# Performance work log

Measured on AMD Instinct MI355X. Metric: run time of the kernel, lower is better.

Reference implementation:

```python
import jax, jax.numpy as jnp
import numpy as np

HIDDEN, FFN, N_EXPERTS, TOP_K = 1024, 2816, 8, 2


def setup_inputs() -> dict:
    key = jax.random.key(0)
    k1, k2, k3, k4, k5 = jax.random.split(key, 5)
    hidden_states = jax.random.normal(k1, (1, 2048, HIDDEN), dtype=jnp.float32)
    # torch Linear weights: [out, in]; experts stacked on leading E axis
    Wgate = jax.random.normal(k2, (N_EXPERTS, HIDDEN), dtype=jnp.float32) * 0.02
    Wg = jax.random.normal(k3, (N_EXPERTS, FFN, HIDDEN), dtype=jnp.float32) * 0.02
    Wu = jax.random.normal(k4, (N_EXPERTS, FFN, HIDDEN), dtype=jnp.float32) * 0.02
    Wd = jax.random.normal(k5, (N_EXPERTS, HIDDEN, FFN), dtype=jnp.float32) * 0.02
    return {"hidden_states": hidden_states, "Wgate": Wgate, "Wg": Wg, "Wu": Wu, "Wd": Wd}


def reference(hidden_states, Wgate, Wg, Wu, Wd):
    x = hidden_states.reshape(-1, hidden_states.shape[-1])  # [T, H]
    # --- router ---
    logits = jnp.einsum('th,eh->te', x, Wgate)               # [T, E]
    weights = jax.nn.softmax(logits, axis=-1)
    topk_w, topk_i = jax.lax.top_k(weights, TOP_K)           # [T, K]
    topk_w = topk_w / jnp.sum(topk_w, axis=-1, keepdims=True)
    # per-token per-expert combine weight (zero if expert not in top-k)
    comb = jnp.sum(jax.nn.one_hot(topk_i, N_EXPERTS, dtype=x.dtype) * topk_w[..., None], axis=1)  # [T, E]
    # --- all-expert SwiGLU (dense reference for the gather-compute-scatter loop) ---
    g = jnp.einsum('th,efh->tef', x, Wg)                     # [T, E, F]
    u = jnp.einsum('th,efh->tef', x, Wu)
    h = jax.nn.silu(g) * u
    y = jnp.einsum('tef,ehf->teh', h, Wd)                    # [T, E, H]
    out = jnp.einsum('te,teh->th', comb, y)                  # [T, H]
    return out
```

## Files before the change

kernel.cpp:

```cpp
#include <hip/hip_runtime.h>
#include <hip/hip_bf16.h>

#define HIDDEN 1024
#define FFN    2816
#define NEXP   8
#define NTOK   2048

typedef __attribute__((ext_vector_type(8))) short short8;
typedef __attribute__((ext_vector_type(4))) short bf16x4;
typedef __attribute__((ext_vector_type(4))) float f32x4;

static __device__ __forceinline__ short f2bf(float f) {
    __hip_bfloat16 h = __float2bfloat16(f);
    return *(short*)&h;
}

static __device__ __forceinline__ void gl_lds16(const short* g, short* l) {
    __builtin_amdgcn_global_load_lds(
        (const __attribute__((address_space(1))) void*)g,
        (__attribute__((address_space(3))) void*)l, 16, 0, 0);
}

#define WAITV(N) asm volatile("s_waitcnt vmcnt(" #N ")" ::: "memory")
#define BAR()    do { __builtin_amdgcn_s_barrier(); \
                      __builtin_amdgcn_sched_barrier(0); } while (0)

static __device__ __forceinline__ void
router_body(int t, int lane, const float* __restrict__ x,
            const float* __restrict__ Wgate, int* __restrict__ counts,
            int* __restrict__ tok, float* __restrict__ wts)
{
    float acc[NEXP];
#pragma unroll
    for (int e = 0; e < NEXP; e++) acc[e] = 0.f;
    const float* xrow = x + (size_t)t * HIDDEN;
    for (int h = lane; h < HIDDEN; h += 64) {
        float xv = xrow[h];
#pragma unroll
        for (int e = 0; e < NEXP; e++) acc[e] += xv * Wgate[e * HIDDEN + h];
    }
#pragma unroll
    for (int off = 32; off > 0; off >>= 1) {
#pragma unroll
        for (int e = 0; e < NEXP; e++) acc[e] += __shfl_down(acc[e], off);
    }
    if (lane == 0) {
        float mx = acc[0];
#pragma unroll
        for (int e = 1; e < NEXP; e++) mx = fmaxf(mx, acc[e]);
        float p[NEXP];
#pragma unroll
        for (int e = 0; e < NEXP; e++) p[e] = __expf(acc[e] - mx);
        int i0 = 0; float p0 = p[0];
#pragma unroll
        for (int e = 1; e < NEXP; e++) if (p[e] > p0) { p0 = p[e]; i0 = e; }
        int i1 = -1; float p1 = -1.f;
#pragma unroll
        for (int e = 0; e < NEXP; e++) {
            if (e == i0) continue;
            if (p[e] > p1) { p1 = p[e]; i1 = e; }
        }
        float inv = 1.f / (p0 + p1);
        float w0 = p0 * inv, w1 = p1 * inv;
        int s0 = atomicAdd(&counts[i0], 1);
        tok[i0 * NTOK + s0] = t; wts[i0 * NTOK + s0] = w0;
        int s1 = atomicAdd(&counts[i1], 1);
        tok[i1 * NTOK + s1] = t; wts[i1 * NTOK + s1] = w1;
    }
}

__global__ void __launch_bounds__(64)
router_kernel(const float* __restrict__ x, const float* __restrict__ Wgate,
              int* __restrict__ counts, int* __restrict__ tok,
              float* __restrict__ wts)
{
    router_body(blockIdx.x, threadIdx.x, x, Wgate, counts, tok, wts);
}

#define N04  ((long long)NTOK * HIDDEN / 4)
#define NW4  ((long long)NEXP * FFN * HIDDEN / 4)
#define CVTA_BLOCKS 11776
__global__ void __launch_bounds__(256)
cvt_xgu_router(const float* __restrict__ x, const float* __restrict__ Wgate,
               int* __restrict__ counts, int* __restrict__ tok,
               float* __restrict__ wts,
               const float* __restrict__ s1, const float* __restrict__ s2,
               short* __restrict__ d0, short* __restrict__ d1,
               short* __restrict__ d2)
{
    int bid = blockIdx.x;
    int tid = threadIdx.x;
    if (bid < 512) {
        int t = bid * 4 + (tid >> 6);
        router_body(t, tid & 63, x, Wgate, counts, tok, wts);
        return;
    }
    long long base4 = (long long)(bid - 512) * 1024;
#pragma unroll
    for (int p = 0; p < 4; p++) {
        long long i = base4 + p * 256 + tid;
        const float* s; short* d; long long r;
        if (i < N04)            { s = x;  d = d0; r = i; }
        else if (i < N04 + NW4) { s = s1; d = d1; r = i - N04; }
        else                    { s = s2; d = d2; r = i - N04 - NW4; }
        float4 a = ((const float4*)s)[r];
        bf16x4 o;
        o[0] = f2bf(a.x); o[1] = f2bf(a.y); o[2] = f2bf(a.z); o[3] = f2bf(a.w);
        *(bf16x4*)(d + 4 * r) = o;
    }
}

#define FFN1_BLOCKS 2816
#define CVTD_BLOCKS 2048
__global__ void __launch_bounds__(256, 2)
ffn1_v6(const short* __restrict__ xbf, const short* __restrict__ Wgbf,
        const short* __restrict__ Wubf, const int* __restrict__ counts,
        const int* __restrict__ tok, short* __restrict__ hbuf,
        const float* __restrict__ Wd, short* __restrict__ wdbf)
{
    int bid = blockIdx.x;
    int tid = threadIdx.x;
    if (bid >= FFN1_BLOCKS) {
        long long base4 = (long long)(bid - FFN1_BLOCKS) * 2816;
#pragma unroll
        for (int p = 0; p < 11; p++) {
            long long r = base4 + p * 256 + tid;
            float4 a = ((const float4*)Wd)[r];
            bf16x4 o;
            o[0] = f2bf(a.x); o[1] = f2bf(a.y); o[2] = f2bf(a.z); o[3] = f2bf(a.w);
            *(bf16x4*)(wdbf + 4 * r) = o;
        }
        return;
    }
    int xb  = bid / 176;
    int yz  = bid - xb * 176;
    int e   = yz / 22;
    int fb  = yz - e * 22;
    int cnt = counts[e];
    int row0 = xb * 128;
    if (row0 >= cnt) return;
    int off_e = 0;
#pragma unroll
    for (int i = 0; i < NEXP; i++) if (i < e) off_e += counts[i];
    int f0 = fb * 128;

    __shared__ short Xs[3][128 * 32];
    __shared__ short Gs[3][128 * 32];
    __shared__ short Us[3][128 * 32];
    __shared__ int   stok[128];

    if (tid < 128) stok[tid] = tok[e * NTOK + min(row0 + tid, cnt - 1)];
    __syncthreads();

    int lane = tid & 63, w = tid >> 6;
    int l15 = lane & 15, lq = lane >> 4;
    int wm = (w & 1) * 64, wn = (w >> 1) * 64;

    int prow   = lane >> 2;
    int gchunk = (lane & 3) ^ ((lane >> 3) & 3);
    const short* xsrc[2]; const short* gsrc[2]; const short* usrc[2];
    int rb[2];
#pragma unroll
    for (int j = 0; j < 2; j++) {
        int rbase = w * 32 + j * 16;
        int r = rbase + prow;
        xsrc[j] = xbf + (size_t)stok[r] * HIDDEN + gchunk * 8;
        gsrc[j] = Wgbf + (size_t)e * FFN * HIDDEN + (size_t)(f0 + r) * HIDDEN + gchunk * 8;
        usrc[j] = Wubf + (size_t)e * FFN * HIDDEN + (size_t)(f0 + r) * HIDDEN + gchunk * 8;
        rb[j] = rbase * 32;
    }

    int aoff[4], boff[4];
#pragma unroll
    for (int mi = 0; mi < 4; mi++) {
        int r = wm + mi * 16 + l15;
        aoff[mi] = r * 32 + (lq ^ ((r >> 1) & 3)) * 8;
    }
#pragma unroll
    for (int ni = 0; ni < 4; ni++) {
        int r = wn + ni * 16 + l15;
        boff[ni] = r * 32 + (lq ^ ((r >> 1) & 3)) * 8;
    }

    f32x4 cg[4][4], cu[4][4];
#pragma unroll
    for (int i = 0; i < 4; i++)
#pragma unroll
        for (int j = 0; j < 4; j++) { cg[i][j] = (f32x4)0.f; cu[i][j] = (f32x4)0.f; }

#define STAGE1(B, T) do { int _k = (T) * 32;                       \
    _Pragma("unroll")                                              \
    for (int j = 0; j < 2; j++) {                                  \
        gl_lds16(xsrc[j] + _k, &Xs[B][rb[j]]);                     \
        gl_lds16(gsrc[j] + _k, &Gs[B][rb[j]]);                     \
        gl_lds16(usrc[j] + _k, &Us[B][rb[j]]);                     \
    } } while (0)

#define COMP1(B) do {                                              \
    short8 af[4], bg[4], bu[4];                                    \
    _Pragma("unroll")                                              \
    for (int mi = 0; mi < 4; mi++)                                 \
        af[mi] = *(const short8*)&Xs[B][aoff[mi]];                 \
    _Pragma("unroll")                                              \
    for (int ni = 0; ni < 4; ni++) {                               \
        bg[ni] = *(const short8*)&Gs[B][boff[ni]];                 \
        bu[ni] = *(const short8*)&Us[B][boff[ni]];                 \
    }                                                              \
    _Pragma("unroll")                                              \
    for (int mi = 0; mi < 4; mi++)                                 \
    _Pragma("unroll")                                              \
    for (int ni = 0; ni < 4; ni++) {                               \
        cg[mi][ni] = __builtin_amdgcn_mfma_f32_16x16x32_bf16(af[mi], bg[ni], cg[mi][ni], 0, 0, 0); \
        cu[mi][ni] = __builtin_amdgcn_mfma_f32_16x16x32_bf16(af[mi], bu[ni], cu[mi][ni], 0, 0, 0); \
    } } while (0)

    STAGE1(0, 0); STAGE1(1, 1); STAGE1(2, 2);

    for (int tt = 0; tt < 30; tt += 3) {
        WAITV(12); BAR(); COMP1(0); BAR(); STAGE1(0, tt + 3);
        WAITV(12); BAR(); COMP1(1); BAR(); STAGE1(1, tt + 4);
        WAITV(12); BAR(); COMP1(2); BAR(); if (tt + 5 < 32) STAGE1(2, tt + 5);
    }
    WAITV(6);  BAR(); COMP1(0);
    WAITV(0);  BAR(); COMP1(1);

#undef STAGE1
#undef COMP1

#pragma unroll
    for (int mi = 0; mi < 4; mi++)
#pragma unroll
        for (int r = 0; r < 4; r++) {
            int row = wm + mi * 16 + lq * 4 + r;
            int grow = row0 + row;
            if (grow < cnt) {
                short* hrow = hbuf + (size_t)(off_e + grow) * FFN + f0 + wn;
#pragma unroll
                for (int ni = 0; ni < 4; ni++) {
                    float g = cg[mi][ni][r], u = cu[mi][ni][r];
                    float h = g / (1.f + __expf(-g)) * u;
                    hrow[ni * 16 + l15] = f2bf(h);
                }
            }
        }
}

__global__ void __launch_bounds__(256, 2)
ffn2_v6(const short* __restrict__ hbuf, const short* __restrict__ Wdbf,
        const int* __restrict__ counts, const int* __restrict__ tok,
        const float* __restrict__ wts, float* __restrict__ out)
{
    int bid = blockIdx.x;
    int xb  = bid >> 7;
    int yz  = bid & 127;
    int e   = yz >> 4;
    int y   = yz & 15;
    int cnt = counts[e];
    int row0 = xb * 128;
    if (row0 >= cnt) return;
    int off_e = 0;
#pragma unroll
    for (int i = 0; i < NEXP; i++) if (i < e) off_e += counts[i];
    int h0    = (y >> 1) * 128;
    int kbase = (y & 1) * (FFN / 2);

    __shared__ short Hs[3][128 * 32];
    __shared__ short Ds[3][128 * 32];
    __shared__ int   stok[128];
    __shared__ float swt[128];

    int tid = threadIdx.x;
    if (tid < 128) {
        int rc = min(row0 + tid, cnt - 1);
        stok[tid] = tok[e * NTOK + rc];
        swt[tid]  = wts[e * NTOK + rc];
    }
    __syncthreads();

    int lane = tid & 63, w = tid >> 6;
    int l15 = lane & 15, lq = lane >> 4;
    int wm = (w & 1) * 64, wn = (w >> 1) * 64;

    int prow   = lane >> 2;
    int gchunk = (lane & 3) ^ ((lane >> 3) & 3);
    const short* hsrc[2]; const short* dsrc[2];
    int rb[2];
#pragma unroll
    for (int j = 0; j < 2; j++) {
        int rbase = w * 32 + j * 16;
        int r = rbase + prow;
        hsrc[j] = hbuf + (size_t)(off_e + min(row0 + r, cnt - 1)) * FFN + kbase + gchunk * 8;
        dsrc[j] = Wdbf + (size_t)e * HIDDEN * FFN + (size_t)(h0 + r) * FFN + kbase + gchunk * 8;
        rb[j] = rbase * 32;
    }

    int aoff[4], boff[4];
#pragma unroll
    for (int mi = 0; mi < 4; mi++) {
        int r = wm + mi * 16 + l15;
        aoff[mi] = r * 32 + (lq ^ ((r >> 1) & 3)) * 8;
    }
#pragma unroll
    for (int ni = 0; ni < 4; ni++) {
        int r = wn + ni * 16 + l15;
        boff[ni] = r * 32 + (lq ^ ((r >> 1) & 3)) * 8;
    }

    f32x4 c[4][4];
#pragma unroll
    for (int i = 0; i < 4; i++)
#pragma unroll
        for (int j = 0; j < 4; j++) c[i][j] = (f32x4)0.f;

#define STAGE2(B, T) do { int _k = (T) * 32;                       \
    _Pragma("unroll")                                              \
    for (int j = 0; j < 2; j++) {                                  \
        gl_lds16(hsrc[j] + _k, &Hs[B][rb[j]]);                     \
        gl_lds16(dsrc[j] + _k, &Ds[B][rb[j]]);                     \
    } } while (0)

#define COMP2(B) do {                                              \
    short8 af[4], bd[4];                                           \
    _Pragma("unroll")                                              \
    for (int mi = 0; mi < 4; mi++)                                 \
        af[mi] = *(const short8*)&Hs[B][aoff[mi]];                 \
    _Pragma("unroll")                                              \
    for (int ni = 0; ni < 4; ni++)                                 \
        bd[ni] = *(const short8*)&Ds[B][boff[ni]];                 \
    _Pragma("unroll")                                              \
    for (int mi = 0; mi < 4; mi++)                                 \
    _Pragma("unroll")                                              \
    for (int ni = 0; ni < 4; ni++)                                 \
        c[mi][ni] = __builtin_amdgcn_mfma_f32_16x16x32_bf16(af[mi], bd[ni], c[mi][ni], 0, 0, 0); \
    } while (0)

    STAGE2(0, 0); STAGE2(1, 1); STAGE2(2, 2);

    for (int tt = 0; tt < 42; tt += 3) {
        WAITV(8); BAR(); COMP2(0); BAR(); STAGE2(0, tt + 3);
        WAITV(8); BAR(); COMP2(1); BAR(); STAGE2(1, tt + 4);
        WAITV(8); BAR(); COMP2(2); BAR(); if (tt + 5 < 44) STAGE2(2, tt + 5);
    }
    WAITV(4); BAR(); COMP2(0);
    WAITV(0); BAR(); COMP2(1);

#undef STAGE2
#undef COMP2

#pragma unroll
    for (int mi = 0; mi < 4; mi++)
#pragma unroll
        for (int r = 0; r < 4; r++) {
            int row = wm + mi * 16 + lq * 4 + r;
            int grow = row0 + row;
            if (grow < cnt) {
                int t = stok[row];
                float wgt = swt[row];
                float* orow = out + (size_t)t * HIDDEN + h0 + wn;
#pragma unroll
                for (int ni = 0; ni < 4; ni++)
                    atomicAdd(&orow[ni * 16 + l15], wgt * c[mi][ni][r]);
            }
        }
}

#define LDW 40
__global__ void __launch_bounds__(256, 2)
ffn1_fb(const float* __restrict__ x, const float* __restrict__ Wg,
        const float* __restrict__ Wu, const int* __restrict__ counts,
        const int* __restrict__ tok, __hip_bfloat16* __restrict__ hbuf)
{
    int e = blockIdx.z;
    int cnt = counts[e];
    int row0 = blockIdx.x * 128;
    if (row0 >= cnt) return;
    int off_e = 0;
#pragma unroll
    for (int i = 0; i < NEXP; i++) if (i < e) off_e += counts[i];
    int f0 = blockIdx.y * 64;

    __shared__ short Xs[128][LDW];
    __shared__ short Gs[64][LDW];
    __shared__ short Us[64][LDW];
    __shared__ int   stok[128];

    int tid = threadIdx.x;
    if (tid < 128) stok[tid] = tok[e * NTOK + min(row0 + tid, cnt - 1)];
    __syncthreads();

    int lane = tid & 63, w = tid >> 6;
    int wm = (w & 1) * 64, wn = (w >> 1) * 32;
    int l15 = lane & 15, lq = lane >> 4;

    f32x4 cg[4][2], cu[4][2];
#pragma unroll
    for (int i = 0; i < 4; i++)
#pragma unroll
        for (int j = 0; j < 2; j++) { cg[i][j] = (f32x4)0.f; cu[i][j] = (f32x4)0.f; }

    const float* Wge = Wg + (size_t)e * FFN * HIDDEN;
    const float* Wue = Wu + (size_t)e * FFN * HIDDEN;

    int xr[4], xc[4]; const float* xp[4];
#pragma unroll
    for (int i = 0; i < 4; i++) {
        int idx = tid + 256 * i;
        xr[i] = idx >> 3; xc[i] = (idx & 7) * 4;
        xp[i] = x + (size_t)stok[xr[i]] * HIDDEN + xc[i];
    }
    int wr[2], wc[2]; const float* gp[2]; const float* up[2];
#pragma unroll
    for (int i = 0; i < 2; i++) {
        int idx = tid + 256 * i;
        wr[i] = idx >> 3; wc[i] = (idx & 7) * 4;
        gp[i] = Wge + (size_t)(f0 + wr[i]) * HIDDEN + wc[i];
        up[i] = Wue + (size_t)(f0 + wr[i]) * HIDDEN + wc[i];
    }

    float4 xa[4], ga[2], ua[2];
#pragma unroll
    for (int i = 0; i < 4; i++) xa[i] = *(const float4*)(xp[i]);
#pragma unroll
    for (int i = 0; i < 2; i++) { ga[i] = *(const float4*)(gp[i]); ua[i] = *(const float4*)(up[i]); }

    for (int k0 = 0; k0 < HIDDEN; k0 += 32) {
        __syncthreads();
#pragma unroll
        for (int i = 0; i < 4; i++) {
            short* d = &Xs[xr[i]][xc[i]];
            d[0] = f2bf(xa[i].x); d[1] = f2bf(xa[i].y);
            d[2] = f2bf(xa[i].z); d[3] = f2bf(xa[i].w);
        }
#pragma unroll
        for (int i = 0; i < 2; i++) {
            short* d = &Gs[wr[i]][wc[i]];
            d[0] = f2bf(ga[i].x); d[1] = f2bf(ga[i].y);
            d[2] = f2bf(ga[i].z); d[3] = f2bf(ga[i].w);
            short* d2 = &Us[wr[i]][wc[i]];
            d2[0] = f2bf(ua[i].x); d2[1] = f2bf(ua[i].y);
            d2[2] = f2bf(ua[i].z); d2[3] = f2bf(ua[i].w);
        }
        __syncthreads();
        if (k0 + 32 < HIDDEN) {
            int kn = k0 + 32;
#pragma unroll
            for (int i = 0; i < 4; i++) xa[i] = *(const float4*)(xp[i] + kn);
#pragma unroll
            for (int i = 0; i < 2; i++) { ga[i] = *(const float4*)(gp[i] + kn); ua[i] = *(const float4*)(up[i] + kn); }
        }
        short8 af[4], bg[2], bu[2];
#pragma unroll
        for (int mi = 0; mi < 4; mi++) af[mi] = *(const short8*)&Xs[wm + mi * 16 + l15][lq * 8];
#pragma unroll
        for (int ni = 0; ni < 2; ni++) {
            bg[ni] = *(const short8*)&Gs[wn + ni * 16 + l15][lq * 8];
            bu[ni] = *(const short8*)&Us[wn + ni * 16 + l15][lq * 8];
        }
#pragma unroll
        for (int mi = 0; mi < 4; mi++)
#pragma unroll
            for (int ni = 0; ni < 2; ni++) {
                cg[mi][ni] = __builtin_amdgcn_mfma_f32_16x16x32_bf16(af[mi], bg[ni], cg[mi][ni], 0, 0, 0);
                cu[mi][ni] = __builtin_amdgcn_mfma_f32_16x16x32_bf16(af[mi], bu[ni], cu[mi][ni], 0, 0, 0);
            }
    }

#pragma unroll
    for (int mi = 0; mi < 4; mi++)
#pragma unroll
        for (int r = 0; r < 4; r++) {
            int row = wm + mi * 16 + lq * 4 + r;
            int grow = row0 + row;
            if (grow < cnt) {
                __hip_bfloat16* hrow = hbuf + (size_t)(off_e + grow) * FFN + f0 + wn;
#pragma unroll
                for (int ni = 0; ni < 2; ni++) {
                    float g = cg[mi][ni][r], u = cu[mi][ni][r];
                    float h = g / (1.f + __expf(-g)) * u;
                    hrow[ni * 16 + l15] = __float2bfloat16(h);
                }
            }
        }
}

__global__ void __launch_bounds__(256, 2)
ffn2_fb(const __hip_bfloat16* __restrict__ hbuf, const float* __restrict__ Wd,
        const int* __restrict__ counts, const int* __restrict__ tok,
        const float* __restrict__ wts, float* __restrict__ out)
{
    int e = blockIdx.z;
    int cnt = counts[e];
    int row0 = blockIdx.x * 128;
    if (row0 >= cnt) return;
    int off_e = 0;
#pragma unroll
    for (int i = 0; i < NEXP; i++) if (i < e) off_e += counts[i];
    int h0 = blockIdx.y * 64;

    __shared__ short Hs[128][LDW];
    __shared__ short Ds[64][LDW];
    __shared__ int   stok[128];
    __shared__ float swt[128];

    int tid = threadIdx.x;
    if (tid < 128) {
        int rc = min(row0 + tid, cnt - 1);
        stok[tid] = tok[e * NTOK + rc];
        swt[tid]  = wts[e * NTOK + rc];
    }
    __syncthreads();

    int lane = tid & 63, w = tid >> 6;
    int wm = (w & 1) * 64, wn = (w >> 1) * 32;
    int l15 = lane & 15, lq = lane >> 4;

    f32x4 c[4][2];
#pragma unroll
    for (int i = 0; i < 4; i++)
#pragma unroll
        for (int j = 0; j < 2; j++) c[i][j] = (f32x4)0.f;

    const float* Wde = Wd + (size_t)e * HIDDEN * FFN;

    int hr[2], hc[2]; const short* hp[2];
#pragma unroll
    for (int i = 0; i < 2; i++) {
        int idx = tid + 256 * i;
        hr[i] = idx >> 2; hc[i] = (idx & 3) * 8;
        int ar = min(row0 + hr[i], cnt - 1);
        hp[i] = (const short*)(hbuf + (size_t)(off_e + ar) * FFN + hc[i]);
    }
    int dr[2], dc[2]; const float* dp[2];
#pragma unroll
    for (int i = 0; i < 2; i++) {
        int idx = tid + 256 * i;
        dr[i] = idx >> 3; dc[i] = (idx & 7) * 4;
        dp[i] = Wde + (size_t)(h0 + dr[i]) * FFN + dc[i];
    }

    short8 ha[2]; float4 da[2];
#pragma unroll
    for (int i = 0; i < 2; i++) { ha[i] = *(const short8*)(hp[i]); da[i] = *(const float4*)(dp[i]); }

    for (int k0 = 0; k0 < FFN; k0 += 32) {
        __syncthreads();
#pragma unroll
        for (int i = 0; i < 2; i++) {
            *(short8*)&Hs[hr[i]][hc[i]] = ha[i];
            short* d = &Ds[dr[i]][dc[i]];
            d[0] = f2bf(da[i].x); d[1] = f2bf(da[i].y);
            d[2] = f2bf(da[i].z); d[3] = f2bf(da[i].w);
        }
        __syncthreads();
        if (k0 + 32 < FFN) {
            int kn = k0 + 32;
#pragma unroll
            for (int i = 0; i < 2; i++) { ha[i] = *(const short8*)(hp[i] + kn); da[i] = *(const float4*)(dp[i] + kn); }
        }
        short8 af[4], bf_[2];
#pragma unroll
        for (int mi = 0; mi < 4; mi++) af[mi] = *(const short8*)&Hs[wm + mi * 16 + l15][lq * 8];
#pragma unroll
        for (int ni = 0; ni < 2; ni++) bf_[ni] = *(const short8*)&Ds[wn + ni * 16 + l15][lq * 8];
#pragma unroll
        for (int mi = 0; mi < 4; mi++)
#pragma unroll
            for (int ni = 0; ni < 2; ni++)
                c[mi][ni] = __builtin_amdgcn_mfma_f32_16x16x32_bf16(af[mi], bf_[ni], c[mi][ni], 0, 0, 0);
    }

#pragma unroll
    for (int mi = 0; mi < 4; mi++)
#pragma unroll
        for (int r = 0; r < 4; r++) {
            int row = wm + mi * 16 + lq * 4 + r;
            int grow = row0 + row;
            if (grow < cnt) {
                int t = stok[row];
                float wgt = swt[row];
                float* orow = out + (size_t)t * HIDDEN + h0 + wn;
#pragma unroll
                for (int ni = 0; ni < 2; ni++)
                    atomicAdd(&orow[ni * 16 + l15], wgt * c[mi][ni][r]);
            }
        }
}

extern "C" void kernel_launch(void* const* d_in, const int* in_sizes, int n_in,
                              void* d_out, int out_size, void* d_ws, size_t ws_size,
                              hipStream_t stream) {
    const float* x     = (const float*)d_in[0];
    const float* Wgate = (const float*)d_in[1];
    const float* Wg    = (const float*)d_in[2];
    const float* Wu    = (const float*)d_in[3];
    const float* Wd    = (const float*)d_in[4];
    float* out = (float*)d_out;

    char* ws = (char*)d_ws;
    int*   counts = (int*)ws;
    int*   tok    = (int*)(ws + 256);
    float* wts    = (float*)(ws + 256 + NEXP * NTOK * 4);

    hipMemsetAsync(counts, 0, 256, stream);
    hipMemsetAsync(out, 0, (size_t)out_size * sizeof(float), stream);

    const size_t base = 256 + 2 * (size_t)NEXP * NTOK * 4;
    const size_t NEED = base
        + 2ull * NTOK * HIDDEN
        + 3ull * 2ull * NEXP * FFN * HIDDEN
        + 2ull * 2ull * NTOK * FFN;

    if (ws_size >= NEED) {
        short* xbf  = (short*)(ws + base);
        short* wgbf = xbf  + (size_t)NTOK * HIDDEN;
        short* wubf = wgbf + (size_t)NEXP * FFN * HIDDEN;
        short* wdbf = wubf + (size_t)NEXP * FFN * HIDDEN;
        short* hbuf = wdbf + (size_t)NEXP * HIDDEN * FFN;

        cvt_xgu_router<<<512 + CVTA_BLOCKS, 256, 0, stream>>>(
            x, Wgate, counts, tok, wts, Wg, Wu, xbf, wgbf, wubf);

        ffn1_v6<<<FFN1_BLOCKS + CVTD_BLOCKS, 256, 0, stream>>>(
            xbf, wgbf, wubf, counts, tok, hbuf, Wd, wdbf);

        ffn2_v6<<<2048, 256, 0, stream>>>(hbuf, wdbf, counts, tok, wts, out);
    } else {
        router_kernel<<<NTOK, 64, 0, stream>>>(x, Wgate, counts, tok, wts);
        __hip_bfloat16* hbuf = (__hip_bfloat16*)(ws + base);
        dim3 g1(NTOK / 128, FFN / 64, NEXP);
        ffn1_fb<<<g1, 256, 0, stream>>>(x, Wg, Wu, counts, tok, hbuf);
        dim3 g2(NTOK / 128, HIDDEN / 64, NEXP);
        ffn2_fb<<<g2, 256, 0, stream>>>(hbuf, Wd, counts, tok, wts, out);
    }
}
```

Measured before the change: 448.5 us.

## Convert gate/up weights to bf16 inside ffn1 instead of a separate pass

Removes the standalone fp32-to-bf16 conversion pass over Wg and Wu: ffn1 now loads the fp32 weights into registers, converts them, and writes bf16 tiles to LDS, double-buffered with the x tile DMA. The output zeroing memset is folded into the router/x-convert kernel. This drops a full write and re-read of the bf16 weight copies, but each weight tile is now converted by every token-block that uses it, fp32 reads double the weight traffic inside the GEMM, and pipelining falls from three stages to two.

```diff
diff --git a/kernel.cpp b/kernel.cpp
--- a/kernel.cpp
+++ b/kernel.cpp
@@ -22,6 +22,7 @@
 }
 
 #define WAITV(N) asm volatile("s_waitcnt vmcnt(" #N ")" ::: "memory")
+#define LGKM0    asm volatile("s_waitcnt lgkmcnt(0)" ::: "memory")
 #define BAR()    do { __builtin_amdgcn_s_barrier(); \
                       __builtin_amdgcn_sched_barrier(0); } while (0)
 
@@ -77,44 +78,42 @@
     router_body(blockIdx.x, threadIdx.x, x, Wgate, counts, tok, wts);
 }
 
-#define N04  ((long long)NTOK * HIDDEN / 4)
-#define NW4  ((long long)NEXP * FFN * HIDDEN / 4)
-#define CVTA_BLOCKS 11776
 __global__ void __launch_bounds__(256)
-cvt_xgu_router(const float* __restrict__ x, const float* __restrict__ Wgate,
-               int* __restrict__ counts, int* __restrict__ tok,
-               float* __restrict__ wts,
-               const float* __restrict__ s1, const float* __restrict__ s2,
-               short* __restrict__ d0, short* __restrict__ d1,
-               short* __restrict__ d2)
+fused_rxz(const float* __restrict__ x, const float* __restrict__ Wgate,
+          int* __restrict__ counts, int* __restrict__ tok,
+          float* __restrict__ wts, short* __restrict__ xbf,
+          float* __restrict__ out)
 {
     int bid = blockIdx.x;
     int tid = threadIdx.x;
     if (bid < 512) {
-        int t = bid * 4 + (tid >> 6);
-        router_body(t, tid & 63, x, Wgate, counts, tok, wts);
+        router_body(bid * 4 + (tid >> 6), tid & 63, x, Wgate, counts, tok, wts);
         return;
     }
-    long long base4 = (long long)(bid - 512) * 1024;
-#pragma unroll
-    for (int p = 0; p < 4; p++) {
-        long long i = base4 + p * 256 + tid;
-        const float* s; short* d; long long r;
-        if (i < N04)            { s = x;  d = d0; r = i; }
-        else if (i < N04 + NW4) { s = s1; d = d1; r = i - N04; }
-        else                    { s = s2; d = d2; r = i - N04 - NW4; }
-        float4 a = ((const float4*)s)[r];
-        bf16x4 o;
-        o[0] = f2bf(a.x); o[1] = f2bf(a.y); o[2] = f2bf(a.z); o[3] = f2bf(a.w);
-        *(bf16x4*)(d + 4 * r) = o;
-    }
+    if (bid < 1024) {
+        long long base4 = (long long)(bid - 512) * 1024;
+#pragma unroll
+        for (int p = 0; p < 4; p++) {
+            long long r = base4 + p * 256 + tid;
+            float4 a = ((const float4*)x)[r];
+            bf16x4 o;
+            o[0] = f2bf(a.x); o[1] = f2bf(a.y); o[2] = f2bf(a.z); o[3] = f2bf(a.w);
+            *(bf16x4*)(xbf + 4 * r) = o;
+        }
+        return;
+    }
+    long long base4 = (long long)(bid - 1024) * 1024;
+    float4 z = make_float4(0.f, 0.f, 0.f, 0.f);
+#pragma unroll
+    for (int p = 0; p < 4; p++)
+        ((float4*)out)[base4 + p * 256 + tid] = z;
 }
 
 #define FFN1_BLOCKS 2816
 #define CVTD_BLOCKS 2048
 __global__ void __launch_bounds__(256, 2)
-ffn1_v6(const short* __restrict__ xbf, const short* __restrict__ Wgbf,
-        const short* __restrict__ Wubf, const int* __restrict__ counts,
+ffn1_v7(const short* __restrict__ xbf, const float* __restrict__ Wg,
+        const float* __restrict__ Wu, const int* __restrict__ counts,
         const int* __restrict__ tok, short* __restrict__ hbuf,
         const float* __restrict__ Wd, short* __restrict__ wdbf)
 {
@@ -144,9 +143,9 @@
     for (int i = 0; i < NEXP; i++) if (i < e) off_e += counts[i];
     int f0 = fb * 128;
 
-    __shared__ short Xs[3][128 * 32];
-    __shared__ short Gs[3][128 * 32];
-    __shared__ short Us[3][128 * 32];
+    __shared__ short Xs[2][128 * 32];
+    __shared__ short Gs[2][128 * 32];
+    __shared__ short Us[2][128 * 32];
     __shared__ int   stok[128];
 
     if (tid < 128) stok[tid] = tok[e * NTOK + min(row0 + tid, cnt - 1)];
@@ -158,17 +157,19 @@
 
     int prow   = lane >> 2;
     int gchunk = (lane & 3) ^ ((lane >> 3) & 3);
-    const short* xsrc[2]; const short* gsrc[2]; const short* usrc[2];
+    const short* xsrc[2]; const float* gsrc[2]; const float* usrc[2];
     int rb[2];
 #pragma unroll
     for (int j = 0; j < 2; j++) {
         int rbase = w * 32 + j * 16;
         int r = rbase + prow;
         xsrc[j] = xbf + (size_t)stok[r] * HIDDEN + gchunk * 8;
-        gsrc[j] = Wgbf + (size_t)e * FFN * HIDDEN + (size_t)(f0 + r) * HIDDEN + gchunk * 8;
-        usrc[j] = Wubf + (size_t)e * FFN * HIDDEN + (size_t)(f0 + r) * HIDDEN + gchunk * 8;
+        gsrc[j] = Wg + (size_t)e * FFN * HIDDEN + (size_t)(f0 + r) * HIDDEN + gchunk * 8;
+        usrc[j] = Wu + (size_t)e * FFN * HIDDEN + (size_t)(f0 + r) * HIDDEN + gchunk * 8;
         rb[j] = rbase * 32;
     }
+    int wadr0 = rb[0] + lane * 8;
+    int wadr1 = rb[1] + lane * 8;
 
     int aoff[4], boff[4];
 #pragma unroll
@@ -188,43 +189,83 @@
 #pragma unroll
         for (int j = 0; j < 4; j++) { cg[i][j] = (f32x4)0.f; cu[i][j] = (f32x4)0.f; }
 
-#define STAGE1(B, T) do { int _k = (T) * 32;                       \
-    _Pragma("unroll")                                              \
-    for (int j = 0; j < 2; j++) {                                  \
-        gl_lds16(xsrc[j] + _k, &Xs[B][rb[j]]);                     \
-        gl_lds16(gsrc[j] + _k, &Gs[B][rb[j]]);                     \
-        gl_lds16(usrc[j] + _k, &Us[B][rb[j]]);                     \
+    float4 g0a, g0b, g1a, g1b, u0a, u0b, u1a, u1b;
+
+#define XDMA(B, T) do { int _k = (T) * 32;                          \
+    gl_lds16(xsrc[0] + _k, &Xs[B][rb[0]]);                          \
+    gl_lds16(xsrc[1] + _k, &Xs[B][rb[1]]); } while (0)
+
+#define LOADR(T) do { int _k = (T) * 32;                            \
+    g0a = *(const float4*)(gsrc[0] + _k);                           \
+    g0b = *(const float4*)(gsrc[0] + _k + 4);                       \
+    g1a = *(const float4*)(gsrc[1] + _k);                           \
+    g1b = *(const float4*)(gsrc[1] + _k + 4);                       \
+    u0a = *(const float4*)(usrc[0] + _k);                           \
+    u0b = *(const float4*)(usrc[0] + _k + 4);                       \
+    u1a = *(const float4*)(usrc[1] + _k);                           \
+    u1b = *(const float4*)(usrc[1] + _k + 4); } while (0)
+
+#define PK8(dst, A, Bv) do { short8 _o;                             \
+    _o[0] = f2bf(A.x);  _o[1] = f2bf(A.y);                          \
+    _o[2] = f2bf(A.z);  _o[3] = f2bf(A.w);                          \
+    _o[4] = f2bf(Bv.x); _o[5] = f2bf(Bv.y);                         \
+    _o[6] = f2bf(Bv.z); _o[7] = f2bf(Bv.w);                         \
+    *(short8*)(dst) = _o; } while (0)
+
+#define CVTW(B) do {                                                \
+    PK8(&Gs[B][wadr0], g0a, g0b); PK8(&Gs[B][wadr1], g1a, g1b);     \
+    PK8(&Us[B][wadr0], u0a, u0b); PK8(&Us[B][wadr1], u1a, u1b); } while (0)
+
+#define COMP1(B) do {                                               \
+    short8 af[4];                                                   \
+    _Pragma("unroll")                                               \
+    for (int mi = 0; mi < 4; mi++)                                  \
+        af[mi] = *(const short8*)&Xs[B][aoff[mi]];                  \
+    {   short8 bb[4];                                               \
+        _Pragma("unroll")                                           \
+        for (int ni = 0; ni < 4; ni++)                              \
+            bb[ni] = *(const short8*)&Gs[B][boff[ni]];              \
+        _Pragma("unroll")                                           \
+        for (int mi = 0; mi < 4; mi++)                              \
+        _Pragma("unroll")                                           \
+        for (int ni = 0; ni < 4; ni++)                              \
+            cg[mi][ni] = __builtin_amdgcn_mfma_f32_16x16x32_bf16(af[mi], bb[ni], cg[mi][ni], 0, 0, 0); \
+    }                                                               \
+    {   short8 bb[4];                                               \
+        _Pragma("unroll")                                           \
+        for (int ni = 0; ni < 4; ni++)                              \
+            bb[ni] = *(const short8*)&Us[B][boff[ni]];              \
+        _Pragma("unroll")                                           \
+        for (int mi = 0; mi < 4; mi++)                              \
+        _Pragma("unroll")                                           \
+        for (int ni = 0; ni < 4; ni++)                              \
+            cu[mi][ni] = __builtin_amdgcn_mfma_f32_16x16x32_bf16(af[mi], bb[ni], cu[mi][ni], 0, 0, 0); \
     } } while (0)
 
-#define COMP1(B) do {                                              \
-    short8 af[4], bg[4], bu[4];                                    \
-    _Pragma("unroll")                                              \
-    for (int mi = 0; mi < 4; mi++)                                 \
-        af[mi] = *(const short8*)&Xs[B][aoff[mi]];                 \
-    _Pragma("unroll")                                              \
-    for (int ni = 0; ni < 4; ni++) {                               \
-        bg[ni] = *(const short8*)&Gs[B][boff[ni]];                 \
-        bu[ni] = *(const short8*)&Us[B][boff[ni]];                 \
-    }                                                              \
-    _Pragma("unroll")                                              \
-    for (int mi = 0; mi < 4; mi++)                                 \
-    _Pragma("unroll")                                              \
-    for (int ni = 0; ni < 4; ni++) {                               \
-        cg[mi][ni] = __builtin_amdgcn_mfma_f32_16x16x32_bf16(af[mi], bg[ni], cg[mi][ni], 0, 0, 0); \
-        cu[mi][ni] = __builtin_amdgcn_mfma_f32_16x16x32_bf16(af[mi], bu[ni], cu[mi][ni], 0, 0, 0); \
-    } } while (0)
-
-    STAGE1(0, 0); STAGE1(1, 1); STAGE1(2, 2);
-
-    for (int tt = 0; tt < 30; tt += 3) {
-        WAITV(12); BAR(); COMP1(0); BAR(); STAGE1(0, tt + 3);
-        WAITV(12); BAR(); COMP1(1); BAR(); STAGE1(1, tt + 4);
-        WAITV(12); BAR(); COMP1(2); BAR(); if (tt + 5 < 32) STAGE1(2, tt + 5);
-    }
-    WAITV(6);  BAR(); COMP1(0);
-    WAITV(0);  BAR(); COMP1(1);
-
-#undef STAGE1
+    XDMA(0, 0); LOADR(0);
+
+    for (int tt = 0; tt < 32; tt += 2) {
+        CVTW(0);
+        XDMA(1, tt + 1); LOADR(tt + 1);
+        WAITV(10); LGKM0; BAR();
+        COMP1(0);
+        BAR();
+        CVTW(1);
+        if (tt + 2 < 32) {
+            XDMA(0, tt + 2); LOADR(tt + 2);
+            WAITV(10);
+        } else {
+            WAITV(0);
+        }
+        LGKM0; BAR();
+        COMP1(1);
+        BAR();
+    }
+
+#undef XDMA
+#undef LOADR
+#undef PK8
+#undef CVTW
 #undef COMP1
 
 #pragma unroll
@@ -602,29 +643,26 @@
     float* wts    = (float*)(ws + 256 + NEXP * NTOK * 4);
 
     hipMemsetAsync(counts, 0, 256, stream);
-    hipMemsetAsync(out, 0, (size_t)out_size * sizeof(float), stream);
 
     const size_t base = 256 + 2 * (size_t)NEXP * NTOK * 4;
     const size_t NEED = base
         + 2ull * NTOK * HIDDEN
-        + 3ull * 2ull * NEXP * FFN * HIDDEN
+        + 2ull * NEXP * HIDDEN * FFN
         + 2ull * 2ull * NTOK * FFN;
 
     if (ws_size >= NEED) {
         short* xbf  = (short*)(ws + base);
-        short* wgbf = xbf  + (size_t)NTOK * HIDDEN;
-        short* wubf = wgbf + (size_t)NEXP * FFN * HIDDEN;
-        short* wdbf = wubf + (size_t)NEXP * FFN * HIDDEN;
+        short* wdbf = xbf  + (size_t)NTOK * HIDDEN;
         short* hbuf = wdbf + (size_t)NEXP * HIDDEN * FFN;
 
-        cvt_xgu_router<<<512 + CVTA_BLOCKS, 256, 0, stream>>>(
-            x, Wgate, counts, tok, wts, Wg, Wu, xbf, wgbf, wubf);
-
-        ffn1_v6<<<FFN1_BLOCKS + CVTD_BLOCKS, 256, 0, stream>>>(
-            xbf, wgbf, wubf, counts, tok, hbuf, Wd, wdbf);
+        fused_rxz<<<1536, 256, 0, stream>>>(x, Wgate, counts, tok, wts, xbf, out);
+
+        ffn1_v7<<<FFN1_BLOCKS + CVTD_BLOCKS, 256, 0, stream>>>(
+            xbf, Wg, Wu, counts, tok, hbuf, Wd, wdbf);
 
         ffn2_v6<<<2048, 256, 0, stream>>>(hbuf, wdbf, counts, tok, wts, out);
     } else {
+        hipMemsetAsync(out, 0, (size_t)out_size * sizeof(float), stream);
         router_kernel<<<NTOK, 64, 0, stream>>>(x, Wgate, counts, tok, wts);
         __hip_bfloat16* hbuf = (__hip_bfloat16*)(ws + base);
         dim3 g1(NTOK / 128, FFN / 64, NEXP);
```

Measured after the change: 457.3 us. No clear change (+2.0%).
